# Kernel optimization log

Measured on AMD Instinct MI355X. Metric: run time of the kernel, lower is better.

Reference implementation:

```python
import jax, jax.numpy as jnp
import numpy as np

N = 16384
E = 262144
NODE_DIM = 120
NUM_HEADS = 4
NUM_BASIS = 20
MULS = (64, 32, 16)          # multiplicities of 0e, 1e, 2e
LS = (0, 1, 2)
NUM_IRREPS = 112             # 64+32+16
EQUI_DIM = 240               # 64*1 + 32*3 + 16*5
L_MAX = 2
ATTN_DIM_SCALAR = NODE_DIM // NUM_HEADS        # 30
ATTN_DIM_EQUI = NODE_DIM // (L_MAX + 1)        # 40
SCALE_SCALAR = 1.0 / np.sqrt(NODE_DIM)
SCALE_EQUI = 1.0 / np.sqrt(NUM_IRREPS)
EPS = 1e-5

def _blocks():
    off = 0
    for mul, l in zip(MULS, LS):
        d = 2 * l + 1
        yield off, mul, l, d
        off += mul * d

def equi_dot(x):
    # per-irrep self dot: [E, EQUI_DIM] -> [E, NUM_IRREPS] invariants
    outs = []
    for off, mul, l, d in _blocks():
        blk = x[:, off:off + mul * d].reshape(-1, mul, d)
        outs.append(jnp.sum(blk * blk, axis=-1))
    return jnp.concatenate(outs, axis=1)

def gate_to_components(g):
    # broadcast per-irrep scalar gate [E, NUM_IRREPS] to components [E, EQUI_DIM]
    parts = []
    woff = 0
    for mul, l in zip(MULS, LS):
        d = 2 * l + 1
        parts.append(jnp.repeat(g[:, woff:woff + mul, None], d, axis=-1).reshape(-1, mul * d))
        woff += mul
    return jnp.concatenate(parts, axis=1)

def layer_norm(x, w, b):
    mu = jnp.mean(x, -1, keepdims=True)
    var = jnp.var(x, -1, keepdims=True)
    return (x - mu) * jax.lax.rsqrt(var + EPS) * w + b

def o3_layer_norm(x, w):
    # equivariant layer norm: per irrep block, RMS over (mul, components); mean-center l=0 only
    parts = []
    woff = 0
    for off, mul, l, d in _blocks():
        blk = x[:, off:off + mul * d].reshape(-1, mul, d)
        if l == 0:
            blk = blk - jnp.mean(blk, axis=1, keepdims=True)
        rms = jax.lax.rsqrt(jnp.mean(blk * blk, axis=(1, 2), keepdims=True) + EPS)
        blk = blk * rms * w[woff:woff + mul][None, :, None]
        parts.append(blk.reshape(-1, mul * d))
        woff += mul
    return jnp.concatenate(parts, axis=1)

def mlp(x, w1, b1, w2, b2):
    return jax.nn.silu(x @ w1 + b1) @ w2 + b2

def setup_inputs():
    ks = jax.random.split(jax.random.key(0), 24)
    def lin(k, i, o):
        return jax.random.normal(k, (i, o), jnp.float32) / np.sqrt(i)
    return dict(
        node_scalar=jax.random.normal(ks[0], (N, NODE_DIM), jnp.float32),
        node_equi=jax.random.normal(ks[1], (N, EQUI_DIM), jnp.float32),
        rbf=jax.random.normal(ks[2], (E, NUM_BASIS), jnp.float32),
        fcut=jax.random.uniform(ks[3], (E, 1), jnp.float32),
        rsh=jax.random.normal(ks[4], (E, EQUI_DIM), jnp.float32),
        ln_w=jnp.ones((NODE_DIM,), jnp.float32),
        ln_b=jnp.zeros((NODE_DIM,), jnp.float32),
        o3ln_w=jnp.ones((NUM_IRREPS,), jnp.float32),
        Wq=lin(ks[5], NODE_DIM, NODE_DIM),
        Wk=lin(ks[6], NODE_DIM, NODE_DIM),
        Wv=lin(ks[7], NODE_DIM, NODE_DIM),
        Wqs=lin(ks[8], NODE_DIM, NODE_DIM),
        Wks=lin(ks[9], NODE_DIM, NODE_DIM),
        Wvs=lin(ks[10], NODE_DIM, NUM_IRREPS),
        rbf_w1=lin(ks[11], NUM_BASIS, NODE_DIM),
        rbf_b1=jnp.zeros((NODE_DIM,), jnp.float32),
        rbf_w2=lin(ks[12], NODE_DIM, NODE_DIM),
        rbf_b2=jnp.zeros((NODE_DIM,), jnp.float32),
        inv_w1=lin(ks[13], NUM_IRREPS, NODE_DIM),
        inv_b1=jnp.zeros((NODE_DIM,), jnp.float32),
        inv_w2=lin(ks[14], NODE_DIM, NODE_DIM),
        inv_b2=jnp.zeros((NODE_DIM,), jnp.float32),
        edge_index=jax.random.randint(ks[15], (2, E), 0, N),
    )

def reference(node_scalar, node_equi, rbf, fcut, rsh, ln_w, ln_b, o3ln_w, Wq, Wk, Wv, Wqs, Wks, Wvs, rbf_w1, rbf_b1, rbf_w2, rbf_b2, inv_w1, inv_b1, inv_w2, inv_b2, edge_index):
    center, neighbor = edge_index[0], edge_index[1]
    ns = layer_norm(node_scalar, ln_w, ln_b)
    ne = o3_layer_norm(node_equi, o3ln_w)
    q_inv = ns @ Wq; k_inv = ns @ Wk; v_inv = ns @ Wv
    q_sph = ns @ Wqs; k_sph = ns @ Wks; v_sph = ns @ Wvs
    # EquiFilter: equivariant difference -> per-irrep invariants -> MLP, plus radial MLP
    x_ij = ne[neighbor] - ne[center]
    w_ij = mlp(equi_dot(x_ij), inv_w1, inv_b1, inv_w2, inv_b2) + mlp(rbf, rbf_w1, rbf_b1, rbf_w2, rbf_b2)
    w_ij = w_ij * fcut
    # scalar multi-head dot-product attention (softmax-free)
    q_s = (q_inv[center] * w_ij).reshape(E, NUM_HEADS, ATTN_DIM_SCALAR)
    k_s = k_inv[neighbor].reshape(E, NUM_HEADS, ATTN_DIM_SCALAR)
    v_s = v_inv[neighbor].reshape(E, NUM_HEADS, ATTN_DIM_SCALAR)
    attn_s = jnp.sum(q_s * k_s, -1, keepdims=True) * SCALE_SCALAR
    msg_scalar = (attn_s * v_s).reshape(E, NODE_DIM)
    # equivariant gated attention
    q_e = (q_sph[center] * w_ij).reshape(E, L_MAX + 1, ATTN_DIM_EQUI)
    k_e = k_sph[neighbor].reshape(E, L_MAX + 1, ATTN_DIM_EQUI)
    v_e = v_sph[neighbor]                                   # [E, NUM_IRREPS]
    attn_e = jnp.sum(q_e * k_e, -1) * SCALE_EQUI            # [E, L_MAX+1]
    attn_e = jnp.concatenate([jnp.repeat(attn_e[:, i:i + 1], MULS[i], axis=1) for i in range(L_MAX + 1)], axis=1)
    gate = attn_e * v_e                                     # [E, NUM_IRREPS]
    msg_equi = rsh * gate_to_components(gate) * fcut        # elementwise tensor product with 0e gates
    out_scalar = node_scalar.at[center].add(msg_scalar)
    out_equi = node_equi.at[center].add(msg_equi)
    return out_scalar, out_equi
```

## Files before the change

kernel.cpp:

```cpp
#include <hip/hip_runtime.h>
#include <hip/hip_bf16.h>
#include <hip/hip_fp16.h>

#define N_NODES 16384
#define E_EDGES 262144

#define SCALE_S 0.09128709291752768f
#define SCALE_E 0.09449111825230679f

#define OFF_ACC   256
#define ACC_BYTES ((size_t)N_NODES * 360 * 4)
#define OFF_TAB   (OFF_ACC + ACC_BYTES)
#define OFF_NS    (OFF_TAB + (size_t)N_NODES * 952 * 2)
#define OFF_W1T   (OFF_NS + (size_t)N_NODES * 128 * 2)
#define OFF_W2T   (OFF_W1T + 256 * 160 * 2)
#define OFF_WNT   (OFF_W2T + 128 * 256 * 2)
#define OFF_B1    (OFF_WNT + 768 * 128 * 2)
#define OFF_B2    (OFF_B1 + 1024)
#define OFF_WIJ   (OFF_B2 + 512)

#define OFF_CNT   OFF_ACC
#define OFF_BASE  (OFF_ACC + 65536)
#define OFF_CUR   (OFF_ACC + 131584)
#define OFF_SORT  (OFF_ACC + 197632)
#define SORT_CLR_BYTES 197632

typedef __attribute__((ext_vector_type(8))) short short8;
typedef __attribute__((ext_vector_type(4))) float f32x4;

#define SF_STRIDE 168
#define SB_STRIDE 40
#define TR_STRIDE 40

#define REGION1_BYTES (64 * 240 * 2)
#define SMEM_MLP (64 * SF_STRIDE * 2 + REGION1_BYTES + 64 * 4 + 2 * 64 * 4)

static __device__ __forceinline__ float b2f(short s) {
    return __uint_as_float(((unsigned int)(unsigned short)s) << 16);
}
static __device__ __forceinline__ short f2b(float v) {
    __hip_bfloat16 h = __float2bfloat16(v);
    return *reinterpret_cast<short*>(&h);
}
static __device__ __forceinline__ short f2h(float v) {
    __half h = __float2half(v);
    return *reinterpret_cast<short*>(&h);
}
static __device__ __forceinline__ float h2f(short s) {
    __half h = *reinterpret_cast<__half*>(&s);
    return __half2float(h);
}
static __device__ __forceinline__ float ldin(const void* p, size_t i, int bfm) {
    return bfm ? b2f(((const short*)p)[i]) : ((const float*)p)[i];
}

__global__ void detect_kernel(const unsigned short* __restrict__ lnw_bits, int* __restrict__ flag) {
    if (threadIdx.x == 0 && blockIdx.x == 0)
        *flag = (lnw_bits[0] == 0x3F80u) ? 1 : 0;
}

__global__ __launch_bounds__(256) void hist_kernel(const int* __restrict__ eidx, void* ws) {
    int* cnt = (int*)((char*)ws + OFF_CNT);
    int e = blockIdx.x * 256 + threadIdx.x;
    atomicAdd(&cnt[eidx[e]], 1);
}

__global__ __launch_bounds__(256) void scan_kernel(void* ws) {
    __shared__ int lds[256];
    int* cnt  = (int*)((char*)ws + OFF_CNT);
    int* base = (int*)((char*)ws + OFF_BASE);
    const int t = threadIdx.x;
    int s = 0;
    for (int j = 0; j < 64; ++j) s += cnt[t * 64 + j];
    lds[t] = s;
    __syncthreads();
    for (int off = 1; off < 256; off <<= 1) {
        int add = (t >= off) ? lds[t - off] : 0;
        __syncthreads();
        lds[t] += add;
        __syncthreads();
    }
    int run = lds[t] - s;
    for (int j = 0; j < 64; ++j) {
        int v = cnt[t * 64 + j];
        base[t * 64 + j] = run;
        run += v;
    }
    if (t == 0) base[16384] = E_EDGES;
}

__global__ __launch_bounds__(256) void scatter_kernel(const int* __restrict__ eidx, void* ws) {
    const int* base = (const int*)((char*)ws + OFF_BASE);
    int* cur    = (int*)((char*)ws + OFF_CUR);
    int* sorted = (int*)((char*)ws + OFF_SORT);
    int e = blockIdx.x * 256 + threadIdx.x;
    int c = eidx[e];
    int pos = base[c] + atomicAdd(&cur[c], 1);
    sorted[pos] = e;
}

__global__ __launch_bounds__(256) void prep_kernel(
    const void* inv_w1, const void* rbf_w1, const void* inv_w2, const void* rbf_w2,
    const void* inv_b1, const void* rbf_b1, const void* inv_b2, const void* rbf_b2,
    const void* Wq, const void* Wk, const void* Wv,
    const void* Wqs, const void* Wks, const void* Wvs,
    void* ws, const int* __restrict__ flag)
{
    short* W1T = (short*)((char*)ws + OFF_W1T);
    short* W2T = (short*)((char*)ws + OFF_W2T);
    short* WNT = (short*)((char*)ws + OFF_WNT);
    float* b1c = (float*)((char*)ws + OFF_B1);
    float* b2c = (float*)((char*)ws + OFF_B2);
    const int bfm = *flag;
    int g = blockIdx.x * 256 + threadIdx.x;
    if (g < 40960) {
        int n = g / 160, k = g % 160;
        float v = 0.f;
        if (n < 120 && k < 112) v = ldin(inv_w1, (size_t)k * 120 + n, bfm);
        else if (n >= 120 && n < 240 && k >= 112 && k < 132)
            v = ldin(rbf_w1, (size_t)(k - 112) * 120 + (n - 120), bfm);
        W1T[g] = f2b(v);
    } else if (g < 73728) {
        int g2 = g - 40960;
        int n = g2 / 256, k = g2 % 256;
        float v = 0.f;
        if (n < 120) {
            if (k < 120)      v = ldin(inv_w2, (size_t)k * 120 + n, bfm);
            else if (k < 240) v = ldin(rbf_w2, (size_t)(k - 120) * 120 + n, bfm);
        }
        W2T[g2] = f2b(v);
    } else if (g < 172032) {
        int g3 = g - 73728;
        int n = g3 / 128, k = g3 % 128;
        float v = 0.f;
        if (k < 120) {
            if      (n < 120) v = ldin(Wq,  (size_t)k * 120 + n, bfm);
            else if (n < 240) v = ldin(Wk,  (size_t)k * 120 + (n - 120), bfm);
            else if (n < 360) v = ldin(Wv,  (size_t)k * 120 + (n - 240), bfm);
            else if (n < 480) v = ldin(Wqs, (size_t)k * 120 + (n - 360), bfm);
            else if (n < 600) v = ldin(Wks, (size_t)k * 120 + (n - 480), bfm);
            else if (n < 712) v = ldin(Wvs, (size_t)k * 112 + (n - 600), bfm);
        }
        WNT[g3] = f2b(v);
    } else if (g < 172288) {
        int n = g - 172032;
        b1c[n] = (n < 120) ? ldin(inv_b1, n, bfm) : (n < 240 ? ldin(rbf_b1, n - 120, bfm) : 0.f);
    } else if (g < 172416) {
        int n = g - 172288;
        b2c[n] = (n < 120) ? (ldin(inv_b2, n, bfm) + ldin(rbf_b2, n, bfm)) : 0.f;
    }
}

__global__ __launch_bounds__(256) void nodeln_kernel(
    const void* node_scalar, const void* node_equi,
    const void* ln_w, const void* ln_b, const void* o3ln_w,
    void* ws, const int* __restrict__ flag)
{
    __shared__ float sm[24];
    short* NS  = (short*)((char*)ws + OFF_NS);
    short* tab = (short*)((char*)ws + OFF_TAB);
    const int n = blockIdx.x, t = threadIdx.x, wv = t >> 6, lane = t & 63;
    const int bfm = *flag;

    float xs = (t < 120) ? ldin(node_scalar, (size_t)n * 120 + t, bfm) : 0.f;
    float xe = (t < 240) ? ldin(node_equi, (size_t)n * 240 + t, bfm) : 0.f;

    float a = xs, b = xs * xs, c = (t < 64) ? xe : 0.f;
    #pragma unroll
    for (int m = 1; m < 64; m <<= 1) {
        a += __shfl_xor(a, m);
        b += __shfl_xor(b, m);
        c += __shfl_xor(c, m);
    }
    if (lane == 0) { sm[wv * 3] = a; sm[wv * 3 + 1] = b; sm[wv * 3 + 2] = c; }
    __syncthreads();
    float s  = sm[0] + sm[3] + sm[6] + sm[9];
    float s2 = sm[1] + sm[4] + sm[7] + sm[10];
    float s0 = sm[2] + sm[5] + sm[8] + sm[11];

    float mean = s * (1.f / 120.f);
    float var  = s2 * (1.f / 120.f) - mean * mean;
    float rstd = rsqrtf(var + 1e-5f);
    if (t < 128) {
        float nsv = 0.f;
        if (t < 120) nsv = (xs - mean) * rstd * ldin(ln_w, t, bfm) + ldin(ln_b, t, bfm);
        NS[(size_t)n * 128 + t] = f2b(nsv);
    }

    float mu0 = s0 * (1.f / 64.f);
    float xc  = (t < 64) ? xe - mu0 : xe;
    float p0 = (t < 64) ? xc * xc : 0.f;
    float p1 = (t >= 64 && t < 160) ? xe * xe : 0.f;
    float p2 = (t >= 160 && t < 240) ? xe * xe : 0.f;
    #pragma unroll
    for (int m = 1; m < 64; m <<= 1) {
        p0 += __shfl_xor(p0, m);
        p1 += __shfl_xor(p1, m);
        p2 += __shfl_xor(p2, m);
    }
    if (lane == 0) { sm[12 + wv * 3] = p0; sm[12 + wv * 3 + 1] = p1; sm[12 + wv * 3 + 2] = p2; }
    __syncthreads();
    float ss0 = sm[12] + sm[15] + sm[18] + sm[21];
    float ss1 = sm[13] + sm[16] + sm[19] + sm[22];
    float ss2 = sm[14] + sm[17] + sm[20] + sm[23];

    float r0 = rsqrtf(ss0 * (1.f / 64.f) + 1e-5f);
    float r1 = rsqrtf(ss1 * (1.f / 96.f) + 1e-5f);
    float r2 = rsqrtf(ss2 * (1.f / 80.f) + 1e-5f);
    float nev = 0.f;
    if (t < 64)       nev = xc * r0 * ldin(o3ln_w, t, bfm);
    else if (t < 160) nev = xe * r1 * ldin(o3ln_w, 64 + (t - 64) / 3, bfm);
    else if (t < 240) nev = xe * r2 * ldin(o3ln_w, 96 + (t - 160) / 5, bfm);
    if (t < 240) tab[(size_t)n * 952 + 712 + t] = f2b(nev);
}

__global__ __launch_bounds__(256) void gemm_node_kernel(void* ws)
{
    __shared__ short sA[64 * SB_STRIDE];
    __shared__ short sB[64 * SB_STRIDE];
    const short* NS  = (const short*)((char*)ws + OFF_NS);
    const short* WNT = (const short*)((char*)ws + OFF_WNT);
    short* tab = (short*)((char*)ws + OFF_TAB);

    const int t = threadIdx.x, w = t >> 6, lane = t & 63;
    const int quad = lane >> 4, l15 = lane & 15;
    const int tileM = (blockIdx.x & 255) * 64;
    const int tileN = (blockIdx.x >> 8) * 64;

    f32x4 acc[4];
    for (int i = 0; i < 4; ++i) acc[i] = (f32x4){0.f, 0.f, 0.f, 0.f};

    for (int k0 = 0; k0 < 128; k0 += 32) {
        __syncthreads();
        {
            int row = t >> 2, ch = t & 3;
            *(short8*)&sA[row * SB_STRIDE + ch * 8] =
                *(const short8*)&NS[(size_t)(tileM + row) * 128 + k0 + ch * 8];
            *(short8*)&sB[row * SB_STRIDE + ch * 8] =
                *(const short8*)&WNT[(size_t)(tileN + row) * 128 + k0 + ch * 8];
        }
        __syncthreads();
        short8 a = *(const short8*)&sA[(w * 16 + l15) * SB_STRIDE + quad * 8];
        #pragma unroll
        for (int nt = 0; nt < 4; ++nt) {
            short8 b = *(const short8*)&sB[(nt * 16 + l15) * SB_STRIDE + quad * 8];
            acc[nt] = __builtin_amdgcn_mfma_f32_16x16x32_bf16(a, b, acc[nt], 0, 0, 0);
        }
    }
    #pragma unroll
    for (int nt = 0; nt < 4; ++nt)
        #pragma unroll
        for (int r = 0; r < 4; ++r) {
            int row = tileM + w * 16 + quad * 4 + r;
            int col = tileN + nt * 16 + l15;
            if (col < 712) tab[(size_t)row * 952 + col] = f2b(acc[nt][r]);
        }
}

__global__ __launch_bounds__(256, 3) void mlp_kernel(
    const void* rbf, const void* fcut, const int* __restrict__ eidx,
    void* ws, const int* __restrict__ flag)
{
    extern __shared__ __align__(16) char smem[];
    short* sF   = (short*)smem;
    char*  reg1 = smem + 64 * SF_STRIDE * 2;
    short* sD   = (short*)reg1;
    short* sB   = (short*)reg1;
    short* sTr  = (short*)(reg1 + 256 * SB_STRIDE * 2);
    float* sFc  = (float*)(reg1 + REGION1_BYTES);
    int*   sIC  = (int*)(sFc + 64);
    int*   sIN  = sIC + 64;

    const short* tab = (const short*)((char*)ws + OFF_TAB);
    const short* W1T = (const short*)((char*)ws + OFF_W1T);
    const short* W2T = (const short*)((char*)ws + OFF_W2T);
    const float* b1c = (const float*)((char*)ws + OFF_B1);
    const float* b2c = (const float*)((char*)ws + OFF_B2);
    short* Wij = (short*)((char*)ws + OFF_WIJ);

    const int t = threadIdx.x, w = t >> 6, lane = t & 63;
    const int quad = lane >> 4, l15 = lane & 15;
    const int bfm = *flag;
    const int e0 = blockIdx.x * 64;

    if (t < 64)       sIC[t] = eidx[e0 + t];
    else if (t < 128) sIN[t - 64] = eidx[E_EDGES + e0 + (t - 64)];
    else if (t < 192) sFc[t - 128] = ldin(fcut, e0 + (t - 128), bfm);
    __syncthreads();

    for (int u = t; u < 1920; u += 256) {
        int le = u / 30, ch = u - le * 30;
        const short* pc = tab + (size_t)sIC[le] * 952 + 712 + ch * 8;
        const short* pn = tab + (size_t)sIN[le] * 952 + 712 + ch * 8;
        short8 a = *(const short8*)pc;
        short8 b = *(const short8*)pn;
        short8 s;
        #pragma unroll
        for (int j = 0; j < 8; ++j) {
            float d = b2f(b[j]) - b2f(a[j]);
            s[j] = f2h(d * d);
        }
        *(short8*)&sD[le * 240 + ch * 8] = s;
    }
    __syncthreads();

    for (int u = t; u < 8192; u += 256) {
        int le = u >> 7, ir = u & 127;
        if (ir < 112) {
            const short* p = sD + le * 240;
            float a;
            if (ir < 64) {
                a = h2f(p[ir]);
            } else if (ir < 96) {
                int off = 64 + 3 * (ir - 64);
                a = h2f(p[off]) + h2f(p[off + 1]) + h2f(p[off + 2]);
            } else {
                int off = 160 + 5 * (ir - 96);
                a = h2f(p[off]) + h2f(p[off + 1]) + h2f(p[off + 2])
                  + h2f(p[off + 3]) + h2f(p[off + 4]);
            }
            sF[le * SF_STRIDE + ir] = f2b(a);
        }
    }
    for (int u = t; u < 4096; u += 256) {
        int le = u >> 6, c = u & 63;
        if (c < 48) {
            float v = (c < 20) ? ldin(rbf, (size_t)(e0 + le) * 20 + c, bfm) : 0.f;
            sF[le * SF_STRIDE + 112 + c] = f2b(v);
        }
    }
    __syncthreads();

    f32x4 acc[16];
    #pragma unroll
    for (int i = 0; i < 16; ++i) acc[i] = (f32x4){0.f, 0.f, 0.f, 0.f};
    for (int k0 = 0; k0 < 160; k0 += 32) {
        #pragma unroll
        for (int i = 0; i < 4; ++i) {
            int u = t + i * 256, n = u >> 2, ch = u & 3;
            *(short8*)&sB[n * SB_STRIDE + ch * 8] =
                *(const short8*)&W1T[(size_t)n * 160 + k0 + ch * 8];
        }
        __syncthreads();
        short8 a = *(const short8*)&sF[(w * 16 + l15) * SF_STRIDE + k0 + quad * 8];
        #pragma unroll
        for (int nt = 0; nt < 16; ++nt) {
            short8 b = *(const short8*)&sB[(nt * 16 + l15) * SB_STRIDE + quad * 8];
            acc[nt] = __builtin_amdgcn_mfma_f32_16x16x32_bf16(a, b, acc[nt], 0, 0, 0);
        }
        __syncthreads();
    }

    short* trw = sTr + w * (16 * TR_STRIDE);
    f32x4 acc2[8];
    #pragma unroll
    for (int i = 0; i < 8; ++i) acc2[i] = (f32x4){0.f, 0.f, 0.f, 0.f};
    #pragma unroll
    for (int ks = 0; ks < 8; ++ks) {
        #pragma unroll
        for (int h = 0; h < 2; ++h) {
            int nt = 2 * ks + h;
            float bb = b1c[nt * 16 + l15];
            #pragma unroll
            for (int r = 0; r < 4; ++r) {
                float v = acc[nt][r] + bb;
                v = v / (1.f + __expf(-v));
                trw[(quad * 4 + r) * TR_STRIDE + h * 16 + l15] = f2b(v);
            }
        }
        #pragma unroll
        for (int i = 0; i < 2; ++i) {
            int u = t + i * 256, n = u >> 2, ch = u & 3;
            *(short8*)&sB[n * SB_STRIDE + ch * 8] =
                *(const short8*)&W2T[(size_t)n * 256 + ks * 32 + ch * 8];
        }
        __syncthreads();
        short8 a = *(const short8*)&trw[l15 * TR_STRIDE + quad * 8];
        #pragma unroll
        for (int nt = 0; nt < 8; ++nt) {
            short8 b = *(const short8*)&sB[(nt * 16 + l15) * SB_STRIDE + quad * 8];
            acc2[nt] = __builtin_amdgcn_mfma_f32_16x16x32_bf16(a, b, acc2[nt], 0, 0, 0);
        }
        __syncthreads();
    }

    #pragma unroll
    for (int nt = 0; nt < 8; ++nt)
        #pragma unroll
        for (int r = 0; r < 4; ++r) {
            int lrow = w * 16 + quad * 4 + r;
            int col = nt * 16 + l15;
            float v = (acc2[nt][r] + b2c[col]) * sFc[lrow];
            Wij[(size_t)(e0 + lrow) * 128 + col] = f2b(v);
        }
}

struct ER {
    float wsa, wsb, wea, web, wec;
    float ka, kb, kae, kbe, kce;
    float v0, v1, vs0, vs1, vs2, vs3;
    float r0, r1, r2, r3, fc;
};

__global__ __launch_bounds__(256) void edge2g_kernel(
    const void* node_scalar, const void* node_equi,
    const void* rsh, const void* fcut, const int* __restrict__ eidx,
    void* ws, void* out, const int* __restrict__ flag)
{
    const short* tab = (const short*)((char*)ws + OFF_TAB);
    const short* Wij = (const short*)((char*)ws + OFF_WIJ);
    const int* base   = (const int*)((char*)ws + OFF_BASE);
    const int* sorted = (const int*)((char*)ws + OFF_SORT);

    const int t = threadIdx.x, wvid = t >> 6, lane = t & 63;
    const int c = blockIdx.x * 4 + wvid;
    const int bfm = *flag;
    const short* tc = tab + (size_t)c * 952;

    const int i16 = lane & 15, g = lane >> 4;
    const int ksa = 30 * g + i16;
    const bool vb = (i16 < 14);
    const int ksb = ksa + 16;
    const int kea = 40 * g + i16;
    const bool ge = (g < 3), gec = ge && (i16 < 8);
    const float qs_a = b2f(tc[ksa]);
    const float qs_b = vb ? b2f(tc[ksb]) : 0.f;
    const float qe_a = ge  ? b2f(tc[360 + kea])      : 0.f;
    const float qe_b = ge  ? b2f(tc[360 + kea + 16]) : 0.f;
    const float qe_c = gec ? b2f(tc[360 + kea + 32]) : 0.f;
    const int bs0 = 16 * (lane / 30);
    const int bs1 = 16 * ((lane + 64) / 30);
    const bool jv3 = (lane < 48);
    int wi_[4], be_[4];
    #pragma unroll
    for (int s = 0; s < 4; ++s) {
        int j = lane + 64 * s;
        int wi = 0, le = 0;
        if (j < 64)       { wi = j;                  le = 0; }
        else if (j < 160) { wi = 64 + (j - 64) / 3;  le = 1; }
        else if (j < 240) { wi = 96 + (j - 160) / 5; le = 2; }
        wi_[s] = wi; be_[s] = 16 * le;
    }

    float accS0 = 0.f, accS1 = 0.f;
    float accE0 = 0.f, accE1 = 0.f, accE2 = 0.f, accE3 = 0.f;

    auto loadE = [&](ER& R, int e, int nn) {
        const short* tn = tab + (size_t)nn * 952;
        const short* wr = Wij + (size_t)e * 128;
        R.wsa = b2f(wr[ksa]);
        R.wsb = b2f(wr[ksb]);
        R.ka  = b2f(tn[120 + ksa]);
        R.kb  = b2f(tn[120 + ksb]);
        if (ge) {
            R.wea = b2f(wr[kea]);
            R.web = b2f(wr[kea + 16]);
            R.wec = b2f(wr[kea + 32]);
        } else { R.wea = 0.f; R.web = 0.f; R.wec = 0.f; }
        R.kae = b2f(tn[480 + kea]);
        R.kbe = b2f(tn[480 + kea + 16]);
        R.kce = b2f(tn[480 + kea + 32]);
        R.v0  = b2f(tn[240 + lane]);
        R.v1  = b2f(tn[304 + lane]);
        R.vs0 = b2f(tn[600 + wi_[0]]);
        R.vs1 = b2f(tn[600 + wi_[1]]);
        R.vs2 = b2f(tn[600 + wi_[2]]);
        R.vs3 = b2f(tn[600 + wi_[3]]);
        R.r0  = ldin(rsh, (size_t)e * 240 + lane, bfm);
        R.r1  = ldin(rsh, (size_t)e * 240 + lane + 64, bfm);
        R.r2  = ldin(rsh, (size_t)e * 240 + lane + 128, bfm);
        R.r3  = jv3 ? ldin(rsh, (size_t)e * 240 + lane + 192, bfm) : 0.f;
        R.fc  = ldin(fcut, e, bfm);
    };

    auto computeE = [&](const ER& R) {
        float ps = qs_a * R.wsa * R.ka + qs_b * R.wsb * R.kb;
        float pe = qe_a * R.wea * R.kae + qe_b * R.web * R.kbe + qe_c * R.wec * R.kce;
        #pragma unroll
        for (int m = 1; m < 16; m <<= 1) {
            ps += __shfl_xor(ps, m, 16);
            pe += __shfl_xor(pe, m, 16);
        }
        ps *= SCALE_S;
        pe *= SCALE_E;
        float a0  = __shfl(ps, bs0);
        float a1  = __shfl(ps, bs1);
        float ae0 = __shfl(pe, be_[0]);
        float ae1 = __shfl(pe, be_[1]);
        float ae2 = __shfl(pe, be_[2]);
        float ae3 = __shfl(pe, be_[3]);
        accS0 += a0 * R.v0;
        if (lane < 56) accS1 += a1 * R.v1;
        float fr = R.fc;
        accE0 += ae0 * R.vs0 * R.r0 * fr;
        accE1 += ae1 * R.vs1 * R.r1 * fr;
        accE2 += ae2 * R.vs2 * R.r2 * fr;
        if (jv3) accE3 += ae3 * R.vs3 * R.r3 * fr;
    };

    const int b0v = base[c], b1v = base[c + 1];
    if (b0v < b1v) {
        ER A, B;
        { int e = sorted[b0v]; int nn = eidx[E_EDGES + e]; loadE(A, e, nn); }
        int p = b0v;
        while (true) {
            if (p + 1 < b1v) { int e = sorted[p + 1]; int nn = eidx[E_EDGES + e]; loadE(B, e, nn); }
            computeE(A);
            ++p; if (p >= b1v) break;
            if (p + 1 < b1v) { int e = sorted[p + 1]; int nn = eidx[E_EDGES + e]; loadE(A, e, nn); }
            computeE(B);
            ++p; if (p >= b1v) break;
        }
    }

    const size_t so = (size_t)c * 120;
    {
        float v = ldin(node_scalar, so + lane, bfm) + accS0;
        size_t i = so + lane;
        if (bfm) ((short*)out)[i] = f2b(v); else ((float*)out)[i] = v;
    }
    if (lane < 56) {
        float v = ldin(node_scalar, so + 64 + lane, bfm) + accS1;
        size_t i = so + 64 + lane;
        if (bfm) ((short*)out)[i] = f2b(v); else ((float*)out)[i] = v;
    }
    const size_t eo = (size_t)c * 240;
    const size_t ob = (size_t)N_NODES * 120;
    {
        float v = ldin(node_equi, eo + lane, bfm) + accE0;
        size_t i = ob + eo + lane;
        if (bfm) ((short*)out)[i] = f2b(v); else ((float*)out)[i] = v;
    }
    {
        float v = ldin(node_equi, eo + lane + 64, bfm) + accE1;
        size_t i = ob + eo + lane + 64;
        if (bfm) ((short*)out)[i] = f2b(v); else ((float*)out)[i] = v;
    }
    {
        float v = ldin(node_equi, eo + lane + 128, bfm) + accE2;
        size_t i = ob + eo + lane + 128;
        if (bfm) ((short*)out)[i] = f2b(v); else ((float*)out)[i] = v;
    }
    if (jv3) {
        float v = ldin(node_equi, eo + lane + 192, bfm) + accE3;
        size_t i = ob + eo + lane + 192;
        if (bfm) ((short*)out)[i] = f2b(v); else ((float*)out)[i] = v;
    }
}

extern "C" void kernel_launch(void* const* d_in, const int* in_sizes, int n_in,
                              void* d_out, int out_size, void* d_ws, size_t ws_size,
                              hipStream_t stream) {
    const void* node_scalar = d_in[0];
    const void* node_equi   = d_in[1];
    const void* rbf         = d_in[2];
    const void* fcut        = d_in[3];
    const void* rsh         = d_in[4];
    const void* ln_w        = d_in[5];
    const void* ln_b        = d_in[6];
    const void* o3ln_w      = d_in[7];
    const void* Wq          = d_in[8];
    const void* Wk          = d_in[9];
    const void* Wv          = d_in[10];
    const void* Wqs         = d_in[11];
    const void* Wks         = d_in[12];
    const void* Wvs         = d_in[13];
    const void* rbf_w1      = d_in[14];
    const void* rbf_b1      = d_in[15];
    const void* rbf_w2      = d_in[16];
    const void* rbf_b2      = d_in[17];
    const void* inv_w1      = d_in[18];
    const void* inv_b1      = d_in[19];
    const void* inv_w2      = d_in[20];
    const void* inv_b2      = d_in[21];
    const int*  edge_index  = (const int*)d_in[22];

    int* flag = (int*)d_ws;

    hipFuncSetAttribute(reinterpret_cast<const void*>(mlp_kernel),
                        hipFuncAttributeMaxDynamicSharedMemorySize, SMEM_MLP);

    detect_kernel<<<1, 64, 0, stream>>>((const unsigned short*)ln_w, flag);
    hipMemsetAsync((char*)d_ws + OFF_ACC, 0, SORT_CLR_BYTES, stream);

    hist_kernel<<<E_EDGES / 256, 256, 0, stream>>>(edge_index, d_ws);
    scan_kernel<<<1, 256, 0, stream>>>(d_ws);
    scatter_kernel<<<E_EDGES / 256, 256, 0, stream>>>(edge_index, d_ws);

    prep_kernel<<<674, 256, 0, stream>>>(
        inv_w1, rbf_w1, inv_w2, rbf_w2, inv_b1, rbf_b1, inv_b2, rbf_b2,
        Wq, Wk, Wv, Wqs, Wks, Wvs, d_ws, flag);

    nodeln_kernel<<<N_NODES, 256, 0, stream>>>(
        node_scalar, node_equi, ln_w, ln_b, o3ln_w, d_ws, flag);

    gemm_node_kernel<<<256 * 12, 256, 0, stream>>>(d_ws);

    mlp_kernel<<<E_EDGES / 64, 256, SMEM_MLP, stream>>>(
        rbf, fcut, edge_index, d_ws, flag);

    edge2g_kernel<<<N_NODES / 4, 256, 0, stream>>>(
        node_scalar, node_equi, rsh, fcut, edge_index, d_ws, d_out, flag);
}
```

Baseline: 830.1 us.

## Stage per-edge gathers through LDS with vectorized loads and wave-level index prefetch

```diff
diff --git a/kernel.cpp b/kernel.cpp
--- a/kernel.cpp
+++ b/kernel.cpp
@@ -34,6 +34,8 @@
 
 #define REGION1_BYTES (64 * 240 * 2)
 #define SMEM_MLP (64 * SF_STRIDE * 2 + REGION1_BYTES + 64 * 4 + 2 * 64 * 4)
+
+#define E2_BUF 2432
 
 static __device__ __forceinline__ float b2f(short s) {
     return __uint_as_float(((unsigned int)(unsigned short)s) << 16);
@@ -395,18 +397,15 @@
         }
 }
 
-struct ER {
-    float wsa, wsb, wea, web, wec;
-    float ka, kb, kae, kbe, kce;
-    float v0, v1, vs0, vs1, vs2, vs3;
-    float r0, r1, r2, r3, fc;
-};
+struct SG { int wj; short8 ta; int tb; f32x4 rr; };
 
 __global__ __launch_bounds__(256) void edge2g_kernel(
     const void* node_scalar, const void* node_equi,
     const void* rsh, const void* fcut, const int* __restrict__ eidx,
     void* ws, void* out, const int* __restrict__ flag)
 {
+    __shared__ __align__(16) char sbuf[4][2][E2_BUF];
+
     const short* tab = (const short*)((char*)ws + OFF_TAB);
     const short* Wij = (const short*)((char*)ws + OFF_WIJ);
     const int* base   = (const int*)((char*)ws + OFF_BASE);
@@ -445,37 +444,61 @@
     float accS0 = 0.f, accS1 = 0.f;
     float accE0 = 0.f, accE1 = 0.f, accE2 = 0.f, accE3 = 0.f;
 
-    auto loadE = [&](ER& R, int e, int nn) {
-        const short* tn = tab + (size_t)nn * 952;
-        const short* wr = Wij + (size_t)e * 128;
-        R.wsa = b2f(wr[ksa]);
-        R.wsb = b2f(wr[ksb]);
-        R.ka  = b2f(tn[120 + ksa]);
-        R.kb  = b2f(tn[120 + ksb]);
+    const int b0v = base[c], b1v = base[c + 1];
+    const int deg = b1v - b0v;
+
+    int eL = 0, nnL = 0; float fcL = 0.f;
+    if (lane < deg) {
+        int ee = sorted[b0v + lane];
+        eL = ee;
+        nnL = eidx[E_EDGES + ee];
+        fcL = ldin(fcut, ee, bfm);
+    }
+
+    auto getE = [&](int p, int& e, int& nn, float& fc) {
+        if (p < 64) { e = __shfl(eL, p); nn = __shfl(nnL, p); fc = __shfl(fcL, p); }
+        else {
+            e = sorted[b0v + p];
+            nn = eidx[E_EDGES + e];
+            fc = ldin(fcut, e, bfm);
+        }
+    };
+
+    auto gload = [&](int e, int nn) -> SG {
+        SG L;
+        const int* wr32 = (const int*)(Wij + (size_t)e * 128);
+        L.wj = wr32[lane];
+        const short* tnp = tab + (size_t)nn * 952 + 120;
+        L.ta = ((const short8*)tnp)[lane];
+        L.tb = (lane < 48) ? *(const int*)(tnp + 512 + lane * 2) : 0;
+        if (bfm) {
+            const short* rp = (const short*)rsh + (size_t)e * 240;
+            L.rr = (lane < 30) ? *(const f32x4*)(rp + lane * 8) : (f32x4){0.f,0.f,0.f,0.f};
+        } else {
+            const float* rp = (const float*)rsh + (size_t)e * 240;
+            L.rr = (lane < 60) ? *(const f32x4*)(rp + lane * 4) : (f32x4){0.f,0.f,0.f,0.f};
+        }
+        return L;
+    };
+
+    auto dswrite = [&](char* buf, const SG& L) {
+        ((int*)buf)[lane] = L.wj;
+        *(short8*)(buf + 256 + lane * 16) = L.ta;
+        if (lane < 48) *(int*)(buf + 1280 + lane * 4) = L.tb;
+        if (lane < (bfm ? 30 : 60)) *(f32x4*)(buf + 1472 + lane * 16) = L.rr;
+    };
+
+    auto computeB = [&](const char* buf, float fc) {
+        const short* W = (const short*)buf;
+        const short* T = (const short*)(buf + 256);
+        float ps = qs_a * b2f(W[ksa]) * b2f(T[ksa])
+                 + qs_b * b2f(W[ksb]) * b2f(T[ksb]);
+        float pe = 0.f;
         if (ge) {
-            R.wea = b2f(wr[kea]);
-            R.web = b2f(wr[kea + 16]);
-            R.wec = b2f(wr[kea + 32]);
-        } else { R.wea = 0.f; R.web = 0.f; R.wec = 0.f; }
-        R.kae = b2f(tn[480 + kea]);
-        R.kbe = b2f(tn[480 + kea + 16]);
-        R.kce = b2f(tn[480 + kea + 32]);
-        R.v0  = b2f(tn[240 + lane]);
-        R.v1  = b2f(tn[304 + lane]);
-        R.vs0 = b2f(tn[600 + wi_[0]]);
-        R.vs1 = b2f(tn[600 + wi_[1]]);
-        R.vs2 = b2f(tn[600 + wi_[2]]);
-        R.vs3 = b2f(tn[600 + wi_[3]]);
-        R.r0  = ldin(rsh, (size_t)e * 240 + lane, bfm);
-        R.r1  = ldin(rsh, (size_t)e * 240 + lane + 64, bfm);
-        R.r2  = ldin(rsh, (size_t)e * 240 + lane + 128, bfm);
-        R.r3  = jv3 ? ldin(rsh, (size_t)e * 240 + lane + 192, bfm) : 0.f;
-        R.fc  = ldin(fcut, e, bfm);
-    };
-
-    auto computeE = [&](const ER& R) {
-        float ps = qs_a * R.wsa * R.ka + qs_b * R.wsb * R.kb;
-        float pe = qe_a * R.wea * R.kae + qe_b * R.web * R.kbe + qe_c * R.wec * R.kce;
+            pe = qe_a * b2f(W[kea])      * b2f(T[360 + kea])
+               + qe_b * b2f(W[kea + 16]) * b2f(T[360 + kea + 16])
+               + qe_c * b2f(W[kea + 32]) * b2f(T[360 + kea + 32]);
+        }
         #pragma unroll
         for (int m = 1; m < 16; m <<= 1) {
             ps += __shfl_xor(ps, m, 16);
@@ -489,27 +512,38 @@
         float ae1 = __shfl(pe, be_[1]);
         float ae2 = __shfl(pe, be_[2]);
         float ae3 = __shfl(pe, be_[3]);
-        accS0 += a0 * R.v0;
-        if (lane < 56) accS1 += a1 * R.v1;
-        float fr = R.fc;
-        accE0 += ae0 * R.vs0 * R.r0 * fr;
-        accE1 += ae1 * R.vs1 * R.r1 * fr;
-        accE2 += ae2 * R.vs2 * R.r2 * fr;
-        if (jv3) accE3 += ae3 * R.vs3 * R.r3 * fr;
+        accS0 += a0 * b2f(T[120 + lane]);
+        if (lane < 56) accS1 += a1 * b2f(T[184 + lane]);
+        float r0, r1, r2, r3;
+        if (bfm) {
+            const short* R = (const short*)(buf + 1472);
+            r0 = b2f(R[lane]); r1 = b2f(R[lane + 64]); r2 = b2f(R[lane + 128]);
+            r3 = jv3 ? b2f(R[lane + 192]) : 0.f;
+        } else {
+            const float* R = (const float*)(buf + 1472);
+            r0 = R[lane]; r1 = R[lane + 64]; r2 = R[lane + 128];
+            r3 = jv3 ? R[lane + 192] : 0.f;
+        }
+        accE0 += ae0 * b2f(T[480 + wi_[0]]) * r0 * fc;
+        accE1 += ae1 * b2f(T[480 + wi_[1]]) * r1 * fc;
+        accE2 += ae2 * b2f(T[480 + wi_[2]]) * r2 * fc;
+        if (jv3) accE3 += ae3 * b2f(T[480 + wi_[3]]) * r3 * fc;
     };
 
-    const int b0v = base[c], b1v = base[c + 1];
-    if (b0v < b1v) {
-        ER A, B;
-        { int e = sorted[b0v]; int nn = eidx[E_EDGES + e]; loadE(A, e, nn); }
-        int p = b0v;
-        while (true) {
-            if (p + 1 < b1v) { int e = sorted[p + 1]; int nn = eidx[E_EDGES + e]; loadE(B, e, nn); }
-            computeE(A);
-            ++p; if (p >= b1v) break;
-            if (p + 1 < b1v) { int e = sorted[p + 1]; int nn = eidx[E_EDGES + e]; loadE(A, e, nn); }
-            computeE(B);
-            ++p; if (p >= b1v) break;
+    if (deg > 0) {
+        char* buf0 = sbuf[wvid][0];
+        char* buf1 = sbuf[wvid][1];
+        int e, nn; float fcC, fcN;
+        getE(0, e, nn, fcC);
+        SG L = gload(e, nn);
+        dswrite(buf0, L);
+        for (int p = 0; p < deg; ++p) {
+            char* cur = (p & 1) ? buf1 : buf0;
+            char* nxt = (p & 1) ? buf0 : buf1;
+            bool more = (p + 1 < deg);
+            if (more) { getE(p + 1, e, nn, fcN); L = gload(e, nn); }
+            computeB(cur, fcC);
+            if (more) { dswrite(nxt, L); fcC = fcN; }
         }
     }
 
```

Result: faster. 730.4 us (-12.0%).
